# Kernel tuning notes

Hardware: AMD Instinct MI355X
Metric: run time of the kernel (lower is better)

## Reference

```python
import jax, jax.numpy as jnp
import numpy as np

N_HEAD = 16
N_STATE = 1024
NEG_INF = -1e9


def setup_inputs() -> dict:
    key = jax.random.key(0)
    k1, = jax.random.split(key, 1)
    B, S = 4, 2048
    x = jax.random.normal(k1, (B, S, 3 * N_STATE), dtype=jnp.float32)
    # causal attention mask (1 = keep, 0 = masked), broadcast over heads
    attn_mask = jnp.tril(jnp.ones((S, S), dtype=jnp.float32))[None, None, :, :]
    attn_mask = jnp.broadcast_to(attn_mask, (B, 1, S, S))
    return {"x": x, "attn_mask": attn_mask}


def reference(x, attn_mask) -> jnp.ndarray:
    B, S, _ = x.shape
    d_head = N_STATE // N_HEAD
    q = x[:, :, :N_STATE].reshape(B, S, N_HEAD, d_head).transpose(0, 2, 1, 3)  # [B,H,S,D]
    k = x[:, :, N_STATE:2 * N_STATE].reshape(B, S, N_HEAD, d_head).transpose(0, 2, 1, 3)
    v = x[:, :, 2 * N_STATE:].reshape(B, S, N_HEAD, d_head).transpose(0, 2, 1, 3)
    scale = 1.0 / jnp.sqrt(jnp.asarray(d_head, dtype=x.dtype))
    w = jnp.einsum('bhqd,bhkd->bhqk', q, k) * scale           # [B,H,S,S]
    w = attn_mask * w + (1.0 - attn_mask) * NEG_INF
    w = jax.nn.softmax(w, axis=-1)
    # attention_dropout is identity at inference (Keras Dropout, training=False)
    a = jnp.einsum('bhqk,bhkd->bhqd', w, v)                   # [B,H,S,D]
    return a.transpose(0, 2, 1, 3).reshape(B, S, N_STATE)
```

## Files before the change

kernel.cpp:

```cpp
#include <hip/hip_runtime.h>
#include <hip/hip_bf16.h>


typedef float  f32x4   __attribute__((ext_vector_type(4)));
typedef float  f32x16  __attribute__((ext_vector_type(16)));
typedef short  bf16x8  __attribute__((ext_vector_type(8)));

#define NH      16
#define DH      64
#define SEQ     2048
#define NSTATE  1024
#define ROW3    3072
#define BQ      256
#define BK      64
#define NQB     (SEQ / BQ)
#define KST     72
#define VST     72
#define NEG_BIG (-1e9f)
#define QSC     (0.125f * 1.4426950408889634f)

static __device__ __forceinline__ unsigned pk2(float x, float y) {
    float2 f2; f2.x = x; f2.y = y;
    __hip_bfloat162 b = __float22bfloat162_rn(f2);
    unsigned r;
    __builtin_memcpy(&r, &b, 4);
    return r;
}

#define ISSUE_STAGE(KV0)                                                       \
    {                                                                          \
        _Pragma("unroll")                                                      \
        for (int i = 0; i < 2; ++i) {                                          \
            int p  = tid + 512 * i;                                            \
            int kv = p >> 4;                                                   \
            int d  = (p & 15) * 4;                                             \
            kp[i] = *(const f32x4*)(kbase + (size_t)((KV0) + kv) * ROW3 + d);  \
        }                                                                      \
        _Pragma("unroll")                                                      \
        for (int i = 0; i < 4; ++i) {                                          \
            int d  = (tid & 15) + 16 * i;                                      \
            int kv = (tid >> 4) * 2;                                           \
            const float* gp = vbase + (size_t)((KV0) + kv) * ROW3 + d;         \
            vp[2 * i]     = gp[0];                                             \
            vp[2 * i + 1] = gp[ROW3];                                          \
        }                                                                      \
    }

#define COMMIT_STAGE(BUF)                                                      \
    {                                                                          \
        _Pragma("unroll")                                                      \
        for (int i = 0; i < 2; ++i) {                                          \
            int p  = tid + 512 * i;                                            \
            int kv = p >> 4;                                                   \
            int d  = (p & 15) * 4;                                             \
            uint2 w;                                                           \
            w.x = pk2(kp[i][0], kp[i][1]);                                     \
            w.y = pk2(kp[i][2], kp[i][3]);                                     \
            *(uint2*)&Klds[BUF][kv * KST + d] = w;                             \
        }                                                                      \
        _Pragma("unroll")                                                      \
        for (int i = 0; i < 4; ++i) {                                          \
            int d  = (tid & 15) + 16 * i;                                      \
            int kv = (tid >> 4) * 2;                                           \
            *(unsigned*)&Vlds[BUF][d * VST + kv] = pk2(vp[2 * i], vp[2 * i + 1]); \
        }                                                                      \
    }

__global__ __launch_bounds__(512, 2)
void mha_fwd(const float* __restrict__ x, float* __restrict__ out) {
    const int tid  = threadIdx.x;
    const int wave = tid >> 6;
    const int lane = tid & 63;
    const int r31  = lane & 31;
    const int hl   = lane >> 5;

    const int bid = blockIdx.x;
    const int pr  = bid >> 6;
    const int bh  = bid & 63;
    const int b   = bh >> 4;
    const int h   = bh & 15;

    const float* xb    = x + (size_t)b * SEQ * ROW3;
    const float* kbase = xb + NSTATE + h * DH;
    const float* vbase = xb + 2 * NSTATE + h * DH;
    float*       ob    = out + (size_t)b * SEQ * NSTATE + h * DH;

    __shared__ __align__(16) short Klds[2][BK * KST];
    __shared__ __align__(16) short Vlds[2][DH * VST];

    f32x4 kp[2];
    float vp[8];

#pragma unroll 1
    for (int ph = 0; ph < 2; ++ph) {
        const int qblk   = ph ? (NQB - 1 - pr) : pr;
        const int q0     = qblk * BQ;
        const int qstrip = q0 + wave * 32;
        const int qrow   = qstrip + r31;

        bf16x8 qf[4];
        {
            const float* qp = xb + (size_t)qrow * ROW3 + h * DH + hl * 8;
#pragma unroll
            for (int kc = 0; kc < 4; ++kc) {
                f32x4 a = *(const f32x4*)(qp + 16 * kc);
                f32x4 c = *(const f32x4*)(qp + 16 * kc + 4);
                union { bf16x8 v; unsigned u[4]; } qq;
                qq.u[0] = pk2(a[0] * QSC, a[1] * QSC);
                qq.u[1] = pk2(a[2] * QSC, a[3] * QSC);
                qq.u[2] = pk2(c[0] * QSC, c[1] * QSC);
                qq.u[3] = pk2(c[2] * QSC, c[3] * QSC);
                qf[kc] = qq.v;
            }
        }

        f32x16 o0, o1;
#pragma unroll
        for (int r = 0; r < 16; ++r) { o0[r] = 0.f; o1[r] = 0.f; }
        float dl = 0.f;

        const int ntiles = q0 / BK + BQ / BK;

        __syncthreads();
        ISSUE_STAGE(0)
        COMMIT_STAGE(0)
        __syncthreads();

#pragma unroll 1
        for (int it = 0; it < ntiles; ++it) {
            const int kv0 = it * BK;
            const int cur = it & 1;
            const bool pf = (it + 1 < ntiles);

            if (pf) ISSUE_STAGE((it + 1) * BK)

            if (kv0 <= qstrip + 31) {
#pragma unroll
                for (int H = 0; H < 2; ++H) {
                    const int kvb = kv0 + 32 * H;
                    if (kvb <= qstrip + 31) {
                        bf16x8 kf[4];
#pragma unroll
                        for (int kc = 0; kc < 4; ++kc)
                            kf[kc] = *(const bf16x8*)&Klds[cur][(32 * H + r31) * KST + 16 * kc + 8 * hl];

                        f32x16 s;
#pragma unroll
                        for (int r = 0; r < 16; ++r) s[r] = 0.f;
#pragma unroll
                        for (int kc = 0; kc < 4; ++kc)
                            s = __builtin_amdgcn_mfma_f32_32x32x16_bf16(kf[kc], qf[kc], s, 0, 0, 0);

                        if (kvb + 31 > qstrip) {
#pragma unroll
                            for (int r = 0; r < 16; ++r) {
                                int kvg = kvb + (r & 3) + 8 * (r >> 2) + 4 * hl;
                                if (kvg > qrow) s[r] = NEG_BIG;
                            }
                        }
#pragma unroll
                        for (int r = 0; r < 16; ++r)
                            s[r] = __builtin_amdgcn_exp2f(s[r]);

                        {
                            float a0 = (s[0] + s[1]) + (s[2] + s[3]);
                            float a1 = (s[4] + s[5]) + (s[6] + s[7]);
                            float a2 = (s[8] + s[9]) + (s[10] + s[11]);
                            float a3 = (s[12] + s[13]) + (s[14] + s[15]);
                            dl += (a0 + a1) + (a2 + a3);
                        }

#pragma unroll
                        for (int cc = 0; cc < 2; ++cc) {
                            unsigned wA = pk2(s[8 * cc + 0], s[8 * cc + 1]);
                            unsigned wB = pk2(s[8 * cc + 2], s[8 * cc + 3]);
                            unsigned wC = pk2(s[8 * cc + 4], s[8 * cc + 5]);
                            unsigned wD = pk2(s[8 * cc + 6], s[8 * cc + 7]);
                            __asm__ volatile("v_permlane32_swap_b32 %0, %1"
                                             : "+v"(wA), "+v"(wC));
                            __asm__ volatile("v_permlane32_swap_b32 %0, %1"
                                             : "+v"(wB), "+v"(wD));
                            union { bf16x8 v; unsigned u[4]; } pa;
                            pa.u[0] = wA; pa.u[1] = wB; pa.u[2] = wC; pa.u[3] = wD;

                            const int c = 2 * H + cc;
                            bf16x8 vf0 = *(const bf16x8*)&Vlds[cur][(r31)      * VST + 16 * c + 8 * hl];
                            bf16x8 vf1 = *(const bf16x8*)&Vlds[cur][(32 + r31) * VST + 16 * c + 8 * hl];
                            o0 = __builtin_amdgcn_mfma_f32_32x32x16_bf16(pa.v, vf0, o0, 0, 0, 0);
                            o1 = __builtin_amdgcn_mfma_f32_32x32x16_bf16(pa.v, vf1, o1, 0, 0, 0);
                        }
                    }
                }
            }

            if (pf) COMMIT_STAGE(cur ^ 1)
            __syncthreads();
        }

        {
            unsigned da = __builtin_bit_cast(unsigned, dl);
            unsigned db = da;
            __asm__ volatile("v_permlane32_swap_b32 %0, %1" : "+v"(da), "+v"(db));
            float dtot = __builtin_bit_cast(float, da) + __builtin_bit_cast(float, db);
            float rcp  = 1.0f / dtot;
#pragma unroll
            for (int r = 0; r < 16; ++r) {
                int srcq = (r & 3) + 8 * (r >> 2) + 4 * hl;
                float lr = __builtin_bit_cast(float,
                    __builtin_amdgcn_ds_bpermute(srcq << 2,
                        __builtin_bit_cast(int, rcp)));
                const size_t row = (size_t)(qstrip + srcq) * NSTATE;
                ob[row + r31]      = o0[r] * lr;
                ob[row + 32 + r31] = o1[r] * lr;
            }
        }
    }
}

extern "C" void kernel_launch(void* const* d_in, const int* in_sizes, int n_in,
                              void* d_out, int out_size, void* d_ws, size_t ws_size,
                              hipStream_t stream) {
    const float* x = (const float*)d_in[0];
    float* out = (float*)d_out;
    dim3 grid(4 * NH * (NQB / 2));
    dim3 block(512);
    hipLaunchKernelGGL(mha_fwd, grid, block, 0, stream, x, out);
}
```

Baseline: 216.0 us.

## Give each wave two query strips sharing K fragments, one q-block per workgroup

```diff
diff --git a/kernel.cpp b/kernel.cpp
--- a/kernel.cpp
+++ b/kernel.cpp
@@ -30,16 +30,16 @@
 #define ISSUE_STAGE(KV0)                                                       \
     {                                                                          \
         _Pragma("unroll")                                                      \
-        for (int i = 0; i < 2; ++i) {                                          \
-            int p  = tid + 512 * i;                                            \
+        for (int i = 0; i < 4; ++i) {                                          \
+            int p  = tid + 256 * i;                                            \
             int kv = p >> 4;                                                   \
             int d  = (p & 15) * 4;                                             \
             kp[i] = *(const f32x4*)(kbase + (size_t)((KV0) + kv) * ROW3 + d);  \
         }                                                                      \
         _Pragma("unroll")                                                      \
-        for (int i = 0; i < 4; ++i) {                                          \
-            int d  = (tid & 15) + 16 * i;                                      \
-            int kv = (tid >> 4) * 2;                                           \
+        for (int i = 0; i < 8; ++i) {                                          \
+            int d  = (tid & 15) + 16 * (i & 3);                                \
+            int kv = 2 * ((tid >> 4) + 16 * (i >> 2));                         \
             const float* gp = vbase + (size_t)((KV0) + kv) * ROW3 + d;         \
             vp[2 * i]     = gp[0];                                             \
             vp[2 * i + 1] = gp[ROW3];                                          \
@@ -49,8 +49,8 @@
 #define COMMIT_STAGE(BUF)                                                      \
     {                                                                          \
         _Pragma("unroll")                                                      \
-        for (int i = 0; i < 2; ++i) {                                          \
-            int p  = tid + 512 * i;                                            \
+        for (int i = 0; i < 4; ++i) {                                          \
+            int p  = tid + 256 * i;                                            \
             int kv = p >> 4;                                                   \
             int d  = (p & 15) * 4;                                             \
             uint2 w;                                                           \
@@ -59,14 +59,78 @@
             *(uint2*)&Klds[BUF][kv * KST + d] = w;                             \
         }                                                                      \
         _Pragma("unroll")                                                      \
-        for (int i = 0; i < 4; ++i) {                                          \
-            int d  = (tid & 15) + 16 * i;                                      \
-            int kv = (tid >> 4) * 2;                                           \
+        for (int i = 0; i < 8; ++i) {                                          \
+            int d  = (tid & 15) + 16 * (i & 3);                                \
+            int kv = 2 * ((tid >> 4) + 16 * (i >> 2));                         \
             *(unsigned*)&Vlds[BUF][d * VST + kv] = pk2(vp[2 * i], vp[2 * i + 1]); \
         }                                                                      \
     }
 
-__global__ __launch_bounds__(512, 2)
+#define COMPUTE_STRIP(QF, O0, O1, DL, QSTRIP)                                  \
+    {                                                                          \
+        f32x16 s;                                                              \
+        _Pragma("unroll")                                                      \
+        for (int r = 0; r < 16; ++r) s[r] = 0.f;                               \
+        _Pragma("unroll")                                                      \
+        for (int kc = 0; kc < 4; ++kc)                                         \
+            s = __builtin_amdgcn_mfma_f32_32x32x16_bf16(kf[kc], QF[kc], s, 0, 0, 0); \
+        if (kvb + 31 > (QSTRIP)) {                                             \
+            _Pragma("unroll")                                                  \
+            for (int r = 0; r < 16; ++r) {                                     \
+                int kvg = kvb + (r & 3) + 8 * (r >> 2) + 4 * hl;               \
+                if (kvg > (QSTRIP) + r31) s[r] = NEG_BIG;                      \
+            }                                                                  \
+        }                                                                      \
+        _Pragma("unroll")                                                      \
+        for (int r = 0; r < 16; ++r)                                           \
+            s[r] = __builtin_amdgcn_exp2f(s[r]);                               \
+        {                                                                      \
+            float a0 = (s[0] + s[1]) + (s[2] + s[3]);                          \
+            float a1 = (s[4] + s[5]) + (s[6] + s[7]);                          \
+            float a2 = (s[8] + s[9]) + (s[10] + s[11]);                        \
+            float a3 = (s[12] + s[13]) + (s[14] + s[15]);                      \
+            DL += (a0 + a1) + (a2 + a3);                                       \
+        }                                                                      \
+        _Pragma("unroll")                                                      \
+        for (int cc = 0; cc < 2; ++cc) {                                       \
+            unsigned wA = pk2(s[8 * cc + 0], s[8 * cc + 1]);                   \
+            unsigned wB = pk2(s[8 * cc + 2], s[8 * cc + 3]);                   \
+            unsigned wC = pk2(s[8 * cc + 4], s[8 * cc + 5]);                   \
+            unsigned wD = pk2(s[8 * cc + 6], s[8 * cc + 7]);                   \
+            __asm__ volatile("v_permlane32_swap_b32 %0, %1"                    \
+                             : "+v"(wA), "+v"(wC));                            \
+            __asm__ volatile("v_permlane32_swap_b32 %0, %1"                    \
+                             : "+v"(wB), "+v"(wD));                            \
+            union { bf16x8 v; unsigned u[4]; } pa;                             \
+            pa.u[0] = wA; pa.u[1] = wB; pa.u[2] = wC; pa.u[3] = wD;            \
+            const int c = 2 * H + cc;                                          \
+            bf16x8 vf0 = *(const bf16x8*)&Vlds[cur][(r31)      * VST + 16 * c + 8 * hl]; \
+            bf16x8 vf1 = *(const bf16x8*)&Vlds[cur][(32 + r31) * VST + 16 * c + 8 * hl]; \
+            O0 = __builtin_amdgcn_mfma_f32_32x32x16_bf16(pa.v, vf0, O0, 0, 0, 0); \
+            O1 = __builtin_amdgcn_mfma_f32_32x32x16_bf16(pa.v, vf1, O1, 0, 0, 0); \
+        }                                                                      \
+    }
+
+#define EPILOGUE(O0, O1, DL, QSTRIP)                                           \
+    {                                                                          \
+        unsigned da = __builtin_bit_cast(unsigned, DL);                        \
+        unsigned db = da;                                                      \
+        __asm__ volatile("v_permlane32_swap_b32 %0, %1" : "+v"(da), "+v"(db)); \
+        float dtot = __builtin_bit_cast(float, da) + __builtin_bit_cast(float, db); \
+        float rcp  = 1.0f / dtot;                                              \
+        _Pragma("unroll")                                                      \
+        for (int r = 0; r < 16; ++r) {                                         \
+            int srcq = (r & 3) + 8 * (r >> 2) + 4 * hl;                        \
+            float lr = __builtin_bit_cast(float,                               \
+                __builtin_amdgcn_ds_bpermute(srcq << 2,                        \
+                    __builtin_bit_cast(int, rcp)));                            \
+            const size_t row = (size_t)((QSTRIP) + srcq) * NSTATE;             \
+            ob[row + r31]      = O0[r] * lr;                                   \
+            ob[row + 32 + r31] = O1[r] * lr;                                   \
+        }                                                                      \
+    }
+
+__global__ __launch_bounds__(256, 2)
 void mha_fwd(const float* __restrict__ x, float* __restrict__ out) {
     const int tid  = threadIdx.x;
     const int wave = tid >> 6;
@@ -74,11 +138,11 @@
     const int r31  = lane & 31;
     const int hl   = lane >> 5;
 
-    const int bid = blockIdx.x;
-    const int pr  = bid >> 6;
-    const int bh  = bid & 63;
-    const int b   = bh >> 4;
-    const int h   = bh & 15;
+    const int bid  = blockIdx.x;
+    const int qblk = 7 - (bid >> 6);
+    const int bh   = bid & 63;
+    const int b    = bh >> 4;
+    const int h    = bh & 15;
 
     const float* xb    = x + (size_t)b * SEQ * ROW3;
     const float* kbase = xb + NSTATE + h * DH;
@@ -88,133 +152,78 @@
     __shared__ __align__(16) short Klds[2][BK * KST];
     __shared__ __align__(16) short Vlds[2][DH * VST];
 
-    f32x4 kp[2];
-    float vp[8];
+    f32x4 kp[4];
+    float vp[16];
+
+    const int q0  = qblk * BQ;
+    const int qsA = q0 + wave * 64;
+    const int qsB = qsA + 32;
+
+    bf16x8 qfA[4], qfB[4];
+    {
+        const float* qpA = xb + (size_t)(qsA + r31) * ROW3 + h * DH + hl * 8;
+        const float* qpB = xb + (size_t)(qsB + r31) * ROW3 + h * DH + hl * 8;
+#pragma unroll
+        for (int kc = 0; kc < 4; ++kc) {
+            f32x4 a = *(const f32x4*)(qpA + 16 * kc);
+            f32x4 c = *(const f32x4*)(qpA + 16 * kc + 4);
+            union { bf16x8 v; unsigned u[4]; } qq;
+            qq.u[0] = pk2(a[0] * QSC, a[1] * QSC);
+            qq.u[1] = pk2(a[2] * QSC, a[3] * QSC);
+            qq.u[2] = pk2(c[0] * QSC, c[1] * QSC);
+            qq.u[3] = pk2(c[2] * QSC, c[3] * QSC);
+            qfA[kc] = qq.v;
+            a = *(const f32x4*)(qpB + 16 * kc);
+            c = *(const f32x4*)(qpB + 16 * kc + 4);
+            qq.u[0] = pk2(a[0] * QSC, a[1] * QSC);
+            qq.u[1] = pk2(a[2] * QSC, a[3] * QSC);
+            qq.u[2] = pk2(c[0] * QSC, c[1] * QSC);
+            qq.u[3] = pk2(c[2] * QSC, c[3] * QSC);
+            qfB[kc] = qq.v;
+        }
+    }
+
+    f32x16 oA0, oA1, oB0, oB1;
+#pragma unroll
+    for (int r = 0; r < 16; ++r) { oA0[r] = 0.f; oA1[r] = 0.f; oB0[r] = 0.f; oB1[r] = 0.f; }
+    float dlA = 0.f, dlB = 0.f;
+
+    const int ntiles = q0 / BK + BQ / BK;
+
+    ISSUE_STAGE(0)
+    COMMIT_STAGE(0)
+    __syncthreads();
 
 #pragma unroll 1
-    for (int ph = 0; ph < 2; ++ph) {
-        const int qblk   = ph ? (NQB - 1 - pr) : pr;
-        const int q0     = qblk * BQ;
-        const int qstrip = q0 + wave * 32;
-        const int qrow   = qstrip + r31;
-
-        bf16x8 qf[4];
-        {
-            const float* qp = xb + (size_t)qrow * ROW3 + h * DH + hl * 8;
-#pragma unroll
-            for (int kc = 0; kc < 4; ++kc) {
-                f32x4 a = *(const f32x4*)(qp + 16 * kc);
-                f32x4 c = *(const f32x4*)(qp + 16 * kc + 4);
-                union { bf16x8 v; unsigned u[4]; } qq;
-                qq.u[0] = pk2(a[0] * QSC, a[1] * QSC);
-                qq.u[1] = pk2(a[2] * QSC, a[3] * QSC);
-                qq.u[2] = pk2(c[0] * QSC, c[1] * QSC);
-                qq.u[3] = pk2(c[2] * QSC, c[3] * QSC);
-                qf[kc] = qq.v;
+    for (int it = 0; it < ntiles; ++it) {
+        const int kv0 = it * BK;
+        const int cur = it & 1;
+        const bool pf = (it + 1 < ntiles);
+
+        if (pf) ISSUE_STAGE((it + 1) * BK)
+
+        if (kv0 <= qsB + 31) {
+#pragma unroll
+            for (int H = 0; H < 2; ++H) {
+                const int kvb = kv0 + 32 * H;
+                if (kvb <= qsB + 31) {
+                    bf16x8 kf[4];
+#pragma unroll
+                    for (int kc = 0; kc < 4; ++kc)
+                        kf[kc] = *(const bf16x8*)&Klds[cur][(32 * H + r31) * KST + 16 * kc + 8 * hl];
+
+                    if (kvb <= qsA + 31) COMPUTE_STRIP(qfA, oA0, oA1, dlA, qsA)
+                    COMPUTE_STRIP(qfB, oB0, oB1, dlB, qsB)
+                }
             }
         }
 
-        f32x16 o0, o1;
-#pragma unroll
-        for (int r = 0; r < 16; ++r) { o0[r] = 0.f; o1[r] = 0.f; }
-        float dl = 0.f;
-
-        const int ntiles = q0 / BK + BQ / BK;
-
+        if (pf) COMMIT_STAGE(cur ^ 1)
         __syncthreads();
-        ISSUE_STAGE(0)
-        COMMIT_STAGE(0)
-        __syncthreads();
-
-#pragma unroll 1
-        for (int it = 0; it < ntiles; ++it) {
-            const int kv0 = it * BK;
-            const int cur = it & 1;
-            const bool pf = (it + 1 < ntiles);
-
-            if (pf) ISSUE_STAGE((it + 1) * BK)
-
-            if (kv0 <= qstrip + 31) {
-#pragma unroll
-                for (int H = 0; H < 2; ++H) {
-                    const int kvb = kv0 + 32 * H;
-                    if (kvb <= qstrip + 31) {
-                        bf16x8 kf[4];
-#pragma unroll
-                        for (int kc = 0; kc < 4; ++kc)
-                            kf[kc] = *(const bf16x8*)&Klds[cur][(32 * H + r31) * KST + 16 * kc + 8 * hl];
-
-                        f32x16 s;
-#pragma unroll
-                        for (int r = 0; r < 16; ++r) s[r] = 0.f;
-#pragma unroll
-                        for (int kc = 0; kc < 4; ++kc)
-                            s = __builtin_amdgcn_mfma_f32_32x32x16_bf16(kf[kc], qf[kc], s, 0, 0, 0);
-
-                        if (kvb + 31 > qstrip) {
-#pragma unroll
-                            for (int r = 0; r < 16; ++r) {
-                                int kvg = kvb + (r & 3) + 8 * (r >> 2) + 4 * hl;
-                                if (kvg > qrow) s[r] = NEG_BIG;
-                            }
-                        }
-#pragma unroll
-                        for (int r = 0; r < 16; ++r)
-                            s[r] = __builtin_amdgcn_exp2f(s[r]);
-
-                        {
-                            float a0 = (s[0] + s[1]) + (s[2] + s[3]);
-                            float a1 = (s[4] + s[5]) + (s[6] + s[7]);
-                            float a2 = (s[8] + s[9]) + (s[10] + s[11]);
-                            float a3 = (s[12] + s[13]) + (s[14] + s[15]);
-                            dl += (a0 + a1) + (a2 + a3);
-                        }
-
-#pragma unroll
-                        for (int cc = 0; cc < 2; ++cc) {
-                            unsigned wA = pk2(s[8 * cc + 0], s[8 * cc + 1]);
-                            unsigned wB = pk2(s[8 * cc + 2], s[8 * cc + 3]);
-                            unsigned wC = pk2(s[8 * cc + 4], s[8 * cc + 5]);
-                            unsigned wD = pk2(s[8 * cc + 6], s[8 * cc + 7]);
-                            __asm__ volatile("v_permlane32_swap_b32 %0, %1"
-                                             : "+v"(wA), "+v"(wC));
-                            __asm__ volatile("v_permlane32_swap_b32 %0, %1"
-                                             : "+v"(wB), "+v"(wD));
-                            union { bf16x8 v; unsigned u[4]; } pa;
-                            pa.u[0] = wA; pa.u[1] = wB; pa.u[2] = wC; pa.u[3] = wD;
-
-                            const int c = 2 * H + cc;
-                            bf16x8 vf0 = *(const bf16x8*)&Vlds[cur][(r31)      * VST + 16 * c + 8 * hl];
-                            bf16x8 vf1 = *(const bf16x8*)&Vlds[cur][(32 + r31) * VST + 16 * c + 8 * hl];
-                            o0 = __builtin_amdgcn_mfma_f32_32x32x16_bf16(pa.v, vf0, o0, 0, 0, 0);
-                            o1 = __builtin_amdgcn_mfma_f32_32x32x16_bf16(pa.v, vf1, o1, 0, 0, 0);
-                        }
-                    }
-                }
-            }
-
-            if (pf) COMMIT_STAGE(cur ^ 1)
-            __syncthreads();
-        }
-
-        {
-            unsigned da = __builtin_bit_cast(unsigned, dl);
-            unsigned db = da;
-            __asm__ volatile("v_permlane32_swap_b32 %0, %1" : "+v"(da), "+v"(db));
-            float dtot = __builtin_bit_cast(float, da) + __builtin_bit_cast(float, db);
-            float rcp  = 1.0f / dtot;
-#pragma unroll
-            for (int r = 0; r < 16; ++r) {
-                int srcq = (r & 3) + 8 * (r >> 2) + 4 * hl;
-                float lr = __builtin_bit_cast(float,
-                    __builtin_amdgcn_ds_bpermute(srcq << 2,
-                        __builtin_bit_cast(int, rcp)));
-                const size_t row = (size_t)(qstrip + srcq) * NSTATE;
-                ob[row + r31]      = o0[r] * lr;
-                ob[row + 32 + r31] = o1[r] * lr;
-            }
-        }
-    }
+    }
+
+    EPILOGUE(oA0, oA1, dlA, qsA)
+    EPILOGUE(oB0, oB1, dlB, qsB)
 }
 
 extern "C" void kernel_launch(void* const* d_in, const int* in_sizes, int n_in,
@@ -222,7 +231,7 @@
                               hipStream_t stream) {
     const float* x = (const float*)d_in[0];
     float* out = (float*)d_out;
-    dim3 grid(4 * NH * (NQB / 2));
-    dim3 block(512);
+    dim3 grid(NQB * 4 * NH);
+    dim3 block(256);
     hipLaunchKernelGGL(mha_fwd, grid, block, 0, stream, x, out);
 }
```

Result: slower. 233.9 us (+8.3%).

## Precompute bf16 K/V in MFMA-fragment layout and drop LDS staging

Applied to the files above, without the earlier changes.

```diff
diff --git a/kernel.cpp b/kernel.cpp
--- a/kernel.cpp
+++ b/kernel.cpp
@@ -11,13 +11,10 @@
 #define SEQ     2048
 #define NSTATE  1024
 #define ROW3    3072
-#define BQ      256
-#define BK      64
-#define NQB     (SEQ / BQ)
-#define KST     72
-#define VST     72
 #define NEG_BIG (-1e9f)
 #define QSC     (0.125f * 1.4426950408889634f)
+#define BH_ELEMS 131072
+#define VOFF_WS  8388608
 
 static __device__ __forceinline__ unsigned pk2(float x, float y) {
     float2 f2; f2.x = x; f2.y = y;
@@ -27,192 +24,164 @@
     return r;
 }
 
-#define ISSUE_STAGE(KV0)                                                       \
-    {                                                                          \
-        _Pragma("unroll")                                                      \
-        for (int i = 0; i < 2; ++i) {                                          \
-            int p  = tid + 512 * i;                                            \
-            int kv = p >> 4;                                                   \
-            int d  = (p & 15) * 4;                                             \
-            kp[i] = *(const f32x4*)(kbase + (size_t)((KV0) + kv) * ROW3 + d);  \
-        }                                                                      \
-        _Pragma("unroll")                                                      \
-        for (int i = 0; i < 4; ++i) {                                          \
-            int d  = (tid & 15) + 16 * i;                                      \
-            int kv = (tid >> 4) * 2;                                           \
-            const float* gp = vbase + (size_t)((KV0) + kv) * ROW3 + d;         \
-            vp[2 * i]     = gp[0];                                             \
-            vp[2 * i + 1] = gp[ROW3];                                          \
-        }                                                                      \
+__global__ __launch_bounds__(512)
+void mha_prep(const float* __restrict__ x, short* __restrict__ ws) {
+    const int tid = threadIdx.x;
+    const int bid = blockIdx.x;
+    const int bh  = bid & 63;
+    const int kv0 = (bid >> 6) * 64;
+    const int b = bh >> 4, h = bh & 15;
+
+    const float* kb = x + (size_t)b * SEQ * ROW3 + NSTATE + h * DH;
+    const float* vb = x + (size_t)b * SEQ * ROW3 + 2 * NSTATE + h * DH;
+    short* wsK = ws + (size_t)bh * BH_ELEMS;
+    short* wsV = ws + VOFF_WS + (size_t)bh * BH_ELEMS;
+
+    __shared__ __align__(16) short Vt[DH * 72];
+
+#pragma unroll
+    for (int i = 0; i < 2; ++i) {
+        int p  = tid + 512 * i;
+        int kv = p >> 4;
+        int d0 = (p & 15) * 4;
+        f32x4 v = *(const f32x4*)(kb + (size_t)(kv0 + kv) * ROW3 + d0);
+        uint2 w;
+        w.x = pk2(v[0], v[1]);
+        w.y = pk2(v[2], v[3]);
+        int kc = d0 >> 4, hl = (d0 >> 3) & 1;
+        *(uint2*)&wsK[((kc * 2 + hl) * 2048 + kv0 + kv) * 8 + (d0 & 7)] = w;
     }
+#pragma unroll
+    for (int i = 0; i < 4; ++i) {
+        int d  = (tid & 15) + 16 * i;
+        int kv = (tid >> 4) * 2;
+        const float* gp = vb + (size_t)(kv0 + kv) * ROW3 + d;
+        *(unsigned*)&Vt[d * 72 + kv] = pk2(gp[0], gp[ROW3]);
+    }
+    __syncthreads();
+    {
+        int kvb = tid >> 6;
+        int d   = tid & 63;
+        bf16x8 v = *(const bf16x8*)&Vt[d * 72 + kvb * 8];
+        *(bf16x8*)&wsV[(((kv0 >> 3) + kvb) * 64 + d) * 8] = v;
+    }
+}
 
-#define COMMIT_STAGE(BUF)                                                      \
-    {                                                                          \
-        _Pragma("unroll")                                                      \
-        for (int i = 0; i < 2; ++i) {                                          \
-            int p  = tid + 512 * i;                                            \
-            int kv = p >> 4;                                                   \
-            int d  = (p & 15) * 4;                                             \
-            uint2 w;                                                           \
-            w.x = pk2(kp[i][0], kp[i][1]);                                     \
-            w.y = pk2(kp[i][2], kp[i][3]);                                     \
-            *(uint2*)&Klds[BUF][kv * KST + d] = w;                             \
-        }                                                                      \
-        _Pragma("unroll")                                                      \
-        for (int i = 0; i < 4; ++i) {                                          \
-            int d  = (tid & 15) + 16 * i;                                      \
-            int kv = (tid >> 4) * 2;                                           \
-            *(unsigned*)&Vlds[BUF][d * VST + kv] = pk2(vp[2 * i], vp[2 * i + 1]); \
-        }                                                                      \
-    }
-
-__global__ __launch_bounds__(512, 2)
-void mha_fwd(const float* __restrict__ x, float* __restrict__ out) {
+__global__ __launch_bounds__(256, 4)
+void mha_fwd(const float* __restrict__ x, const short* __restrict__ ws,
+             float* __restrict__ out) {
     const int tid  = threadIdx.x;
-    const int wave = tid >> 6;
+    const int w    = tid >> 6;
     const int lane = tid & 63;
     const int r31  = lane & 31;
     const int hl   = lane >> 5;
 
-    const int bid = blockIdx.x;
-    const int pr  = bid >> 6;
-    const int bh  = bid & 63;
-    const int b   = bh >> 4;
-    const int h   = bh & 15;
+    const int bid   = blockIdx.x;
+    const int bh    = bid & 63;
+    const int g     = bid >> 6;
+    const int strip = 4 * (15 - g) + w;
+    const int b = bh >> 4, h = bh & 15;
 
-    const float* xb    = x + (size_t)b * SEQ * ROW3;
-    const float* kbase = xb + NSTATE + h * DH;
-    const float* vbase = xb + 2 * NSTATE + h * DH;
-    float*       ob    = out + (size_t)b * SEQ * NSTATE + h * DH;
+    const float* xb  = x + (size_t)b * SEQ * ROW3;
+    float*       ob  = out + (size_t)b * SEQ * NSTATE + h * DH;
+    const short* wsK = ws + (size_t)bh * BH_ELEMS;
+    const short* wsV = ws + VOFF_WS + (size_t)bh * BH_ELEMS;
 
-    __shared__ __align__(16) short Klds[2][BK * KST];
-    __shared__ __align__(16) short Vlds[2][DH * VST];
+    const int qs   = strip * 32;
+    const int qrow = qs + r31;
 
-    f32x4 kp[2];
-    float vp[8];
+    bf16x8 qf[4];
+    {
+        const float* qp = xb + (size_t)qrow * ROW3 + h * DH + hl * 8;
+#pragma unroll
+        for (int kc = 0; kc < 4; ++kc) {
+            f32x4 a = *(const f32x4*)(qp + 16 * kc);
+            f32x4 c = *(const f32x4*)(qp + 16 * kc + 4);
+            union { bf16x8 v; unsigned u[4]; } qq;
+            qq.u[0] = pk2(a[0] * QSC, a[1] * QSC);
+            qq.u[1] = pk2(a[2] * QSC, a[3] * QSC);
+            qq.u[2] = pk2(c[0] * QSC, c[1] * QSC);
+            qq.u[3] = pk2(c[2] * QSC, c[3] * QSC);
+            qf[kc] = qq.v;
+        }
+    }
+
+    f32x16 o0, o1;
+#pragma unroll
+    for (int r = 0; r < 16; ++r) { o0[r] = 0.f; o1[r] = 0.f; }
+    float dl = 0.f;
 
 #pragma unroll 1
-    for (int ph = 0; ph < 2; ++ph) {
-        const int qblk   = ph ? (NQB - 1 - pr) : pr;
-        const int q0     = qblk * BQ;
-        const int qstrip = q0 + wave * 32;
-        const int qrow   = qstrip + r31;
+    for (int kvb = 0; kvb <= qs; kvb += 32) {
+        bf16x8 kf[4];
+#pragma unroll
+        for (int kc = 0; kc < 4; ++kc)
+            kf[kc] = *(const bf16x8*)&wsK[((kc * 2 + hl) * 2048 + kvb + r31) * 8];
+        bf16x8 vfa[2], vfb[2];
+#pragma unroll
+        for (int cc = 0; cc < 2; ++cc) {
+            const int kvblk = (kvb >> 3) + 2 * cc + hl;
+            vfa[cc] = *(const bf16x8*)&wsV[(kvblk * 64 + r31) * 8];
+            vfb[cc] = *(const bf16x8*)&wsV[(kvblk * 64 + 32 + r31) * 8];
+        }
 
-        bf16x8 qf[4];
-        {
-            const float* qp = xb + (size_t)qrow * ROW3 + h * DH + hl * 8;
+        f32x16 s;
 #pragma unroll
-            for (int kc = 0; kc < 4; ++kc) {
-                f32x4 a = *(const f32x4*)(qp + 16 * kc);
-                f32x4 c = *(const f32x4*)(qp + 16 * kc + 4);
-                union { bf16x8 v; unsigned u[4]; } qq;
-                qq.u[0] = pk2(a[0] * QSC, a[1] * QSC);
-                qq.u[1] = pk2(a[2] * QSC, a[3] * QSC);
-                qq.u[2] = pk2(c[0] * QSC, c[1] * QSC);
-                qq.u[3] = pk2(c[2] * QSC, c[3] * QSC);
-                qf[kc] = qq.v;
+        for (int r = 0; r < 16; ++r) s[r] = 0.f;
+#pragma unroll
+        for (int kc = 0; kc < 4; ++kc)
+            s = __builtin_amdgcn_mfma_f32_32x32x16_bf16(kf[kc], qf[kc], s, 0, 0, 0);
+
+        if (kvb == qs) {
+#pragma unroll
+            for (int r = 0; r < 16; ++r) {
+                int kvg = kvb + (r & 3) + 8 * (r >> 2) + 4 * hl;
+                if (kvg > qrow) s[r] = NEG_BIG;
             }
         }
+#pragma unroll
+        for (int r = 0; r < 16; ++r)
+            s[r] = __builtin_amdgcn_exp2f(s[r]);
 
-        f32x16 o0, o1;
-#pragma unroll
-        for (int r = 0; r < 16; ++r) { o0[r] = 0.f; o1[r] = 0.f; }
-        float dl = 0.f;
-
-        const int ntiles = q0 / BK + BQ / BK;
-
-        __syncthreads();
-        ISSUE_STAGE(0)
-        COMMIT_STAGE(0)
-        __syncthreads();
-
-#pragma unroll 1
-        for (int it = 0; it < ntiles; ++it) {
-            const int kv0 = it * BK;
-            const int cur = it & 1;
-            const bool pf = (it + 1 < ntiles);
-
-            if (pf) ISSUE_STAGE((it + 1) * BK)
-
-            if (kv0 <= qstrip + 31) {
-#pragma unroll
-                for (int H = 0; H < 2; ++H) {
-                    const int kvb = kv0 + 32 * H;
-                    if (kvb <= qstrip + 31) {
-                        bf16x8 kf[4];
-#pragma unroll
-                        for (int kc = 0; kc < 4; ++kc)
-                            kf[kc] = *(const bf16x8*)&Klds[cur][(32 * H + r31) * KST + 16 * kc + 8 * hl];
-
-                        f32x16 s;
-#pragma unroll
-                        for (int r = 0; r < 16; ++r) s[r] = 0.f;
-#pragma unroll
-                        for (int kc = 0; kc < 4; ++kc)
-                            s = __builtin_amdgcn_mfma_f32_32x32x16_bf16(kf[kc], qf[kc], s, 0, 0, 0);
-
-                        if (kvb + 31 > qstrip) {
-#pragma unroll
-                            for (int r = 0; r < 16; ++r) {
-                                int kvg = kvb + (r & 3) + 8 * (r >> 2) + 4 * hl;
-                                if (kvg > qrow) s[r] = NEG_BIG;
-                            }
-                        }
-#pragma unroll
-                        for (int r = 0; r < 16; ++r)
-                            s[r] = __builtin_amdgcn_exp2f(s[r]);
-
-                        {
-                            float a0 = (s[0] + s[1]) + (s[2] + s[3]);
-                            float a1 = (s[4] + s[5]) + (s[6] + s[7]);
-                            float a2 = (s[8] + s[9]) + (s[10] + s[11]);
-                            float a3 = (s[12] + s[13]) + (s[14] + s[15]);
-                            dl += (a0 + a1) + (a2 + a3);
-                        }
+        {
+            float a0 = (s[0] + s[1]) + (s[2] + s[3]);
+            float a1 = (s[4] + s[5]) + (s[6] + s[7]);
+            float a2 = (s[8] + s[9]) + (s[10] + s[11]);
+            float a3 = (s[12] + s[13]) + (s[14] + s[15]);
+            dl += (a0 + a1) + (a2 + a3);
+        }
 
 #pragma unroll
-                        for (int cc = 0; cc < 2; ++cc) {
-                            unsigned wA = pk2(s[8 * cc + 0], s[8 * cc + 1]);
-                            unsigned wB = pk2(s[8 * cc + 2], s[8 * cc + 3]);
-                            unsigned wC = pk2(s[8 * cc + 4], s[8 * cc + 5]);
-                            unsigned wD = pk2(s[8 * cc + 6], s[8 * cc + 7]);
-                            __asm__ volatile("v_permlane32_swap_b32 %0, %1"
-                                             : "+v"(wA), "+v"(wC));
-                            __asm__ volatile("v_permlane32_swap_b32 %0, %1"
-                                             : "+v"(wB), "+v"(wD));
-                            union { bf16x8 v; unsigned u[4]; } pa;
-                            pa.u[0] = wA; pa.u[1] = wB; pa.u[2] = wC; pa.u[3] = wD;
+        for (int cc = 0; cc < 2; ++cc) {
+            unsigned wA = pk2(s[8 * cc + 0], s[8 * cc + 1]);
+            unsigned wB = pk2(s[8 * cc + 2], s[8 * cc + 3]);
+            unsigned wC = pk2(s[8 * cc + 4], s[8 * cc + 5]);
+            unsigned wD = pk2(s[8 * cc + 6], s[8 * cc + 7]);
+            __asm__ volatile("v_permlane32_swap_b32 %0, %1" : "+v"(wA), "+v"(wC));
+            __asm__ volatile("v_permlane32_swap_b32 %0, %1" : "+v"(wB), "+v"(wD));
+            union { bf16x8 v; unsigned u[4]; } pa;
+            pa.u[0] = wA; pa.u[1] = wB; pa.u[2] = wC; pa.u[3] = wD;
 
-                            const int c = 2 * H + cc;
-                            bf16x8 vf0 = *(const bf16x8*)&Vlds[cur][(r31)      * VST + 16 * c + 8 * hl];
-                            bf16x8 vf1 = *(const bf16x8*)&Vlds[cur][(32 + r31) * VST + 16 * c + 8 * hl];
-                            o0 = __builtin_amdgcn_mfma_f32_32x32x16_bf16(pa.v, vf0, o0, 0, 0, 0);
-                            o1 = __builtin_amdgcn_mfma_f32_32x32x16_bf16(pa.v, vf1, o1, 0, 0, 0);
-                        }
-                    }
-                }
-            }
+            o0 = __builtin_amdgcn_mfma_f32_32x32x16_bf16(pa.v, vfa[cc], o0, 0, 0, 0);
+            o1 = __builtin_amdgcn_mfma_f32_32x32x16_bf16(pa.v, vfb[cc], o1, 0, 0, 0);
+        }
+    }
 
-            if (pf) COMMIT_STAGE(cur ^ 1)
-            __syncthreads();
-        }
-
-        {
-            unsigned da = __builtin_bit_cast(unsigned, dl);
-            unsigned db = da;
-            __asm__ volatile("v_permlane32_swap_b32 %0, %1" : "+v"(da), "+v"(db));
-            float dtot = __builtin_bit_cast(float, da) + __builtin_bit_cast(float, db);
-            float rcp  = 1.0f / dtot;
+    {
+        unsigned da = __builtin_bit_cast(unsigned, dl);
+        unsigned db = da;
+        __asm__ volatile("v_permlane32_swap_b32 %0, %1" : "+v"(da), "+v"(db));
+        float dtot = __builtin_bit_cast(float, da) + __builtin_bit_cast(float, db);
+        float rcp  = 1.0f / dtot;
 #pragma unroll
-            for (int r = 0; r < 16; ++r) {
-                int srcq = (r & 3) + 8 * (r >> 2) + 4 * hl;
-                float lr = __builtin_bit_cast(float,
-                    __builtin_amdgcn_ds_bpermute(srcq << 2,
-                        __builtin_bit_cast(int, rcp)));
-                const size_t row = (size_t)(qstrip + srcq) * NSTATE;
-                ob[row + r31]      = o0[r] * lr;
-                ob[row + 32 + r31] = o1[r] * lr;
-            }
+        for (int r = 0; r < 16; ++r) {
+            int srcq = (r & 3) + 8 * (r >> 2) + 4 * hl;
+            float lr = __builtin_bit_cast(float,
+                __builtin_amdgcn_ds_bpermute(srcq << 2,
+                    __builtin_bit_cast(int, rcp)));
+            const size_t row = (size_t)(qs + srcq) * NSTATE;
+            ob[row + r31]      = o0[r] * lr;
+            ob[row + 32 + r31] = o1[r] * lr;
         }
     }
 }
@@ -222,7 +191,8 @@
                               hipStream_t stream) {
     const float* x = (const float*)d_in[0];
     float* out = (float*)d_out;
-    dim3 grid(4 * NH * (NQB / 2));
-    dim3 block(512);
-    hipLaunchKernelGGL(mha_fwd, grid, block, 0, stream, x, out);
+    short* ws  = (short*)d_ws;
+
+    hipLaunchKernelGGL(mha_prep, dim3(2048), dim3(512), 0, stream, x, ws);
+    hipLaunchKernelGGL(mha_fwd,  dim3(1024), dim3(256), 0, stream, x, ws, out);
 }
```

Measured after the change: 231.9 us. 1.07x slower.
